# Kernel optimization log

Hardware: AMD Instinct MI355X
Metric: run time of the kernel (lower is better)

Reference implementation:

```python
import jax, jax.numpy as jnp
import numpy as np

N, E, D, L, V = 200000, 500000, 128, 5, 8
BN_EPS = 1e-5


def _bn(h, g, b, m, v):
    # eval-mode BatchNorm1d with running stats
    return (h - m) * jax.lax.rsqrt(v + BN_EPS) * g + b


def setup_inputs() -> dict:
    key = jax.random.key(0)
    ks = iter(jax.random.split(key, 40))
    nk = lambda: next(ks)
    f = lambda shape: jax.random.normal(nk(), shape, jnp.float32) * 0.05
    inp = {}
    inp["x"] = jax.random.normal(nk(), (N, 12), jnp.float32)
    inp["edge_index"] = jax.random.randint(nk(), (2, E), 0, N, dtype=jnp.int32)
    inp["edge_attr"] = jax.random.randint(nk(), (E, 3), 0, V, dtype=jnp.int32)
    # atom encoder: Lin(12,D) -> BN -> ReLU -> Lin(D,D) -> BN -> ReLU -> Lin(D,D)
    inp["ae_W1"] = f((12, D)); inp["ae_b1"] = jnp.zeros((D,), jnp.float32)
    inp["ae_g1"] = jnp.ones((D,), jnp.float32); inp["ae_be1"] = jnp.zeros((D,), jnp.float32)
    inp["ae_m1"] = f((D,)); inp["ae_v1"] = jax.random.uniform(nk(), (D,), jnp.float32) + 0.5
    inp["ae_W2"] = f((D, D)); inp["ae_b2"] = jnp.zeros((D,), jnp.float32)
    inp["ae_g2"] = jnp.ones((D,), jnp.float32); inp["ae_be2"] = jnp.zeros((D,), jnp.float32)
    inp["ae_m2"] = f((D,)); inp["ae_v2"] = jax.random.uniform(nk(), (D,), jnp.float32) + 0.5
    inp["ae_W3"] = f((D, D)); inp["ae_b3"] = jnp.zeros((D,), jnp.float32)
    # per-layer GIN params (stacked over L)
    inp["bond_emb"] = f((L, 3, V, D))
    inp["eps"] = jnp.zeros((L,), jnp.float32)
    inp["mlp_W1"] = f((L, D, D)); inp["mlp_b1"] = jnp.zeros((L, D), jnp.float32)
    inp["mlp_g"] = jnp.ones((L, D), jnp.float32); inp["mlp_be"] = jnp.zeros((L, D), jnp.float32)
    inp["mlp_m"] = f((L, D)); inp["mlp_v"] = jax.random.uniform(nk(), (L, D), jnp.float32) + 0.5
    inp["mlp_W2"] = f((L, D, D)); inp["mlp_b2"] = jnp.zeros((L, D), jnp.float32)
    # per-layer outer BatchNorm
    inp["out_g"] = jnp.ones((L, D), jnp.float32); inp["out_be"] = jnp.zeros((L, D), jnp.float32)
    inp["out_m"] = f((L, D)); inp["out_v"] = jax.random.uniform(nk(), (L, D), jnp.float32) + 0.5
    return inp


def reference(x, edge_index, edge_attr,
              ae_W1, ae_b1, ae_g1, ae_be1, ae_m1, ae_v1,
              ae_W2, ae_b2, ae_g2, ae_be2, ae_m2, ae_v2,
              ae_W3, ae_b3,
              bond_emb, eps, mlp_W1, mlp_b1, mlp_g, mlp_be, mlp_m, mlp_v,
              mlp_W2, mlp_b2, out_g, out_be, out_m, out_v):
    n_nodes = x.shape[0]
    src, dst = edge_index[0], edge_index[1]
    # atom encoder
    h = jax.nn.relu(_bn(x @ ae_W1 + ae_b1, ae_g1, ae_be1, ae_m1, ae_v1))
    h = jax.nn.relu(_bn(h @ ae_W2 + ae_b2, ae_g2, ae_be2, ae_m2, ae_v2))
    h = h @ ae_W3 + ae_b3  # [N, D]
    n_layers = bond_emb.shape[0]
    for l in range(n_layers):
        # BondEncoder: sum of per-feature embeddings -> [E, D]
        be = bond_emb[l]
        e_emb = be[0][edge_attr[:, 0]] + be[1][edge_attr[:, 1]] + be[2][edge_attr[:, 2]]
        # message: relu(x_j + edge_emb); aggregate: scatter-add at dst
        msg = jax.nn.relu(h[src] + e_emb)
        agg = jax.ops.segment_sum(msg, dst, num_segments=n_nodes)
        z = (1.0 + eps[l]) * h + agg
        # GIN MLP: Lin -> BN -> ReLU -> Lin
        z = jax.nn.relu(_bn(z @ mlp_W1[l] + mlp_b1[l], mlp_g[l], mlp_be[l], mlp_m[l], mlp_v[l]))
        z = z @ mlp_W2[l] + mlp_b2[l]
        # outer BatchNorm; ReLU on all but last layer (dropout is identity in eval)
        z = _bn(z, out_g[l], out_be[l], out_m[l], out_v[l])
        if l < n_layers - 1:
            z = jax.nn.relu(z)
        h = z
    return h  # JK='last'
```

## Files before the change

### kernel.cpp

```cpp
#include <hip/hip_runtime.h>
#include <hip/hip_bf16.h>
#include <cstdint>
#include <cstddef>

#define D 128
#define NNODES 200000
#define NEDGES 500000
#define NLAYERS 5
#define BN_EPS 1e-5f
#define MAXDEG 24

typedef __attribute__((ext_vector_type(8))) short bf16x8;
typedef __attribute__((ext_vector_type(4))) float f32x4;

__device__ __forceinline__ unsigned short f2bf(float f) {
    union { float f; unsigned int u; } x; x.f = f;
    unsigned int r = (x.u + 0x7FFFu + ((x.u >> 16) & 1u)) >> 16;
    return (unsigned short)r;
}
__device__ __forceinline__ float bf2f(unsigned short u) {
    union { unsigned int u; float f; } x; x.u = ((unsigned int)u) << 16; return x.f;
}

__global__ void k_zero(int* __restrict__ p, int n) {
    int i = blockIdx.x * 256 + threadIdx.x;
    if (i < n) p[i] = 0;
}

__global__ void k_fill_edges(const int* __restrict__ ei, const int* __restrict__ ea,
                             int* __restrict__ deg, int* __restrict__ elist, int n_edges) {
    int e = blockIdx.x * 256 + threadIdx.x;
    if (e >= n_edges) return;
    int dst = ei[n_edges + e];
    int src = ei[e];
    int a0 = ea[e * 3], a1 = ea[e * 3 + 1], a2 = ea[e * 3 + 2];
    int rec = src | (a0 << 18) | (a1 << 21) | (a2 << 24);
    int pos = atomicAdd(&deg[dst], 1);
    if (pos < MAXDEG) elist[dst * MAXDEG + pos] = rec;
}

__global__ void k_prep_w(const float* __restrict__ aeW2, const float* __restrict__ aeW3,
                         const float* __restrict__ mlpW1, const float* __restrict__ mlpW2,
                         unsigned short* __restrict__ wbt) {
    int m = blockIdx.x >> 3;
    int s = (blockIdx.x & 7) * 256 + threadIdx.x;
    int f = s >> 4;
    int kc = (s & 15) * 8;
    const float* W;
    if (m == 0) W = aeW2;
    else if (m == 1) W = aeW3;
    else if (m < 7) W = mlpW1 + (size_t)(m - 2) * D * D;
    else W = mlpW2 + (size_t)(m - 7) * D * D;
    unsigned short tmp[8];
#pragma unroll
    for (int j = 0; j < 8; ++j) tmp[j] = f2bf(W[(size_t)(kc + j) * D + f]);
    *(int4*)(wbt + (size_t)m * D * D + (size_t)f * D + kc) = *(int4*)tmp;
}

__global__ void k_bondsum(const float* __restrict__ bond, float* __restrict__ bsum) {
    int idx = blockIdx.x;
    int l = idx >> 9, combo = idx & 511;
    int a0 = combo & 7, a1 = (combo >> 3) & 7, a2 = (combo >> 6) & 7;
    int f = threadIdx.x;
    const float* bl = bond + (size_t)l * 3 * 8 * 128;
    bsum[(size_t)idx * 128 + f] =
        bl[a0 * 128 + f] + bl[1024 + a1 * 128 + f] + bl[2048 + a2 * 128 + f];
}

__global__ void k_ae1(const float* __restrict__ x, const float* __restrict__ W,
                      const float* __restrict__ b, const float* __restrict__ g,
                      const float* __restrict__ be, const float* __restrict__ m,
                      const float* __restrict__ v, unsigned short* __restrict__ out) {
    __shared__ float sW[12][128];
    int tid = threadIdx.x;
    for (int i = tid; i < 12 * 128; i += 256) sW[i >> 7][i & 127] = W[i];
    int f0 = (tid & 31) * 4;
    int g8 = tid >> 5;
    float4 bb = *(const float4*)(b + f0);
    float4 gg = *(const float4*)(g + f0);
    float4 ee = *(const float4*)(be + f0);
    float4 mm = *(const float4*)(m + f0);
    float4 vv = *(const float4*)(v + f0);
    float A0 = gg.x * rsqrtf(vv.x + BN_EPS), S0 = (bb.x - mm.x) * A0 + ee.x;
    float A1 = gg.y * rsqrtf(vv.y + BN_EPS), S1 = (bb.y - mm.y) * A1 + ee.y;
    float A2 = gg.z * rsqrtf(vv.z + BN_EPS), S2 = (bb.z - mm.z) * A2 + ee.z;
    float A3 = gg.w * rsqrtf(vv.w + BN_EPS), S3 = (bb.w - mm.w) * A3 + ee.w;
    __syncthreads();
    for (int n = blockIdx.x * 8 + g8; n < NNODES; n += gridDim.x * 8) {
        const float4* xr = (const float4*)(x + (size_t)n * 12);
        float4 x0 = xr[0], x1 = xr[1], x2 = xr[2];
        float xv[12] = {x0.x, x0.y, x0.z, x0.w, x1.x, x1.y, x1.z, x1.w,
                        x2.x, x2.y, x2.z, x2.w};
        float a0 = 0.f, a1 = 0.f, a2 = 0.f, a3 = 0.f;
#pragma unroll
        for (int k = 0; k < 12; ++k) {
            float4 wv = *(float4*)&sW[k][f0];
            a0 += xv[k] * wv.x; a1 += xv[k] * wv.y;
            a2 += xv[k] * wv.z; a3 += xv[k] * wv.w;
        }
        unsigned short o[4];
        o[0] = f2bf(fmaxf(a0 * A0 + S0, 0.f));
        o[1] = f2bf(fmaxf(a1 * A1 + S1, 0.f));
        o[2] = f2bf(fmaxf(a2 * A2 + S2, 0.f));
        o[3] = f2bf(fmaxf(a3 * A3 + S3, 0.f));
        *(uint2*)(out + (size_t)n * D + f0) = *(uint2*)o;
    }
}

__global__ void k_agg(const unsigned short* __restrict__ hin,
                      const float* __restrict__ bsum,
                      const float* __restrict__ eps_arr, int layer,
                      const int* __restrict__ deg, const int* __restrict__ elist,
                      unsigned short* __restrict__ out) {
    int tid = threadIdx.x;
    int f4 = tid & 31;
    int n = blockIdx.x * 8 + (tid >> 5);
    float epsv = 1.f + eps_arr[layer];
    ushort4 hs = *(const ushort4*)(hin + (size_t)n * D + f4 * 4);
    float z0 = epsv * bf2f(hs.x), z1 = epsv * bf2f(hs.y);
    float z2 = epsv * bf2f(hs.z), z3 = epsv * bf2f(hs.w);
    int dgr = min(deg[n], MAXDEG);
    int rec = (f4 < MAXDEG) ? elist[(size_t)n * MAXDEG + f4] : 0;
    for (int base = 0; base < dgr; base += 4) {
        int rr[4];
#pragma unroll
        for (int j = 0; j < 4; ++j) rr[j] = __shfl(rec, base + j, 32);
        ushort4 hv[4]; float4 bv[4];
#pragma unroll
        for (int j = 0; j < 4; ++j) {
            if (base + j < dgr) {
                hv[j] = *(const ushort4*)(hin + (size_t)(rr[j] & 0x3FFFF) * D + f4 * 4);
                bv[j] = *(const float4*)(bsum + (size_t)((rr[j] >> 18) & 511) * D + f4 * 4);
            }
        }
#pragma unroll
        for (int j = 0; j < 4; ++j) {
            if (base + j < dgr) {
                z0 += fmaxf(bf2f(hv[j].x) + bv[j].x, 0.f);
                z1 += fmaxf(bf2f(hv[j].y) + bv[j].y, 0.f);
                z2 += fmaxf(bf2f(hv[j].z) + bv[j].z, 0.f);
                z3 += fmaxf(bf2f(hv[j].w) + bv[j].w, 0.f);
            }
        }
    }
    unsigned short o[4] = {f2bf(z0), f2bf(z1), f2bf(z2), f2bf(z3)};
    *(uint2*)(out + (size_t)n * D + f4 * 4) = *(uint2*)o;
}

#define SWZ(row, bytecol) (((row) * 256 + (bytecol)) ^ (((row) & 7) << 4))
template<int OUTF32>
__launch_bounds__(512, 4)
__global__ void k_mlp2(const unsigned short* __restrict__ hin,
                       const unsigned short* __restrict__ W1t,
                       const float* __restrict__ b1,
                       const float* __restrict__ g1, const float* __restrict__ be1,
                       const float* __restrict__ m1, const float* __restrict__ v1,
                       const unsigned short* __restrict__ W2t,
                       const float* __restrict__ b2,
                       const float* __restrict__ g2, const float* __restrict__ be2,
                       const float* __restrict__ m2, const float* __restrict__ v2,
                       unsigned short* __restrict__ outb, float* __restrict__ outf,
                       int do_bn2, int do_relu2) {
    __shared__ char lds[65536];
    char* sW = lds;
    char* sA = lds + 32768;
    int tid = threadIdx.x;
    size_t nb = (size_t)blockIdx.x * 128;

#pragma unroll
    for (int i = 0; i < 4; ++i) {
        int s = tid + i * 512;
        int r = s >> 4, cc = (s & 15) * 16;
        int4 av = *(const int4*)((const char*)hin + (nb + r) * 256 + cc);
        *(int4*)(sA + SWZ(r, cc)) = av;
        int4 wv = *(const int4*)((const char*)W1t + r * 256 + cc);
        *(int4*)(sW + SWZ(r, cc)) = wv;
    }
    __syncthreads();

    int lane = tid & 63;
    int w = tid >> 6;
    int arow = lane & 15;
    int kq = (lane >> 4) * 8;
    int c = w * 16 + arow;

    f32x4 acc[8];
#pragma unroll
    for (int rt = 0; rt < 8; ++rt) acc[rt] = (f32x4){0.f, 0.f, 0.f, 0.f};
#pragma unroll
    for (int kb = 0; kb < 4; ++kb) {
        int k0 = kb * 32 + kq;
        bf16x8 bf = *(bf16x8*)(sW + SWZ(c, k0 * 2));
#pragma unroll
        for (int rt = 0; rt < 8; ++rt) {
            bf16x8 a = *(bf16x8*)(sA + SWZ(rt * 16 + arow, k0 * 2));
            acc[rt] = __builtin_amdgcn_mfma_f32_16x16x32_bf16(a, bf, acc[rt], 0, 0, 0);
        }
    }
    __syncthreads();

    {
        float sc = g1[c] * rsqrtf(v1[c] + BN_EPS);
        float sh = (b1[c] - m1[c]) * sc + be1[c];
#pragma unroll
        for (int rt = 0; rt < 8; ++rt) {
#pragma unroll
            for (int r = 0; r < 4; ++r) {
                int row = rt * 16 + (lane >> 4) * 4 + r;
                float z = fmaxf(acc[rt][r] * sc + sh, 0.f);
                *(unsigned short*)(sA + SWZ(row, c * 2)) = f2bf(z);
            }
        }
    }
#pragma unroll
    for (int i = 0; i < 4; ++i) {
        int s = tid + i * 512;
        int r = s >> 4, cc = (s & 15) * 16;
        *(int4*)(sW + SWZ(r, cc)) = *(const int4*)((const char*)W2t + r * 256 + cc);
    }
    __syncthreads();

#pragma unroll
    for (int rt = 0; rt < 8; ++rt) acc[rt] = (f32x4){0.f, 0.f, 0.f, 0.f};
#pragma unroll
    for (int kb = 0; kb < 4; ++kb) {
        int k0 = kb * 32 + kq;
        bf16x8 bf = *(bf16x8*)(sW + SWZ(c, k0 * 2));
#pragma unroll
        for (int rt = 0; rt < 8; ++rt) {
            bf16x8 a = *(bf16x8*)(sA + SWZ(rt * 16 + arow, k0 * 2));
            acc[rt] = __builtin_amdgcn_mfma_f32_16x16x32_bf16(a, bf, acc[rt], 0, 0, 0);
        }
    }

    float sc2 = 1.f, sh2;
    if (do_bn2) { sc2 = g2[c] * rsqrtf(v2[c] + BN_EPS); sh2 = (b2[c] - m2[c]) * sc2 + be2[c]; }
    else sh2 = b2[c];
    if constexpr (OUTF32) {
#pragma unroll
        for (int rt = 0; rt < 8; ++rt) {
#pragma unroll
            for (int r = 0; r < 4; ++r) {
                int row = rt * 16 + (lane >> 4) * 4 + r;
                float z = acc[rt][r] * sc2 + sh2;
                if (do_relu2) z = fmaxf(z, 0.f);
                if (nb + row < NNODES) outf[(nb + row) * D + c] = z;
            }
        }
    } else {
        __syncthreads();
#pragma unroll
        for (int rt = 0; rt < 8; ++rt) {
#pragma unroll
            for (int r = 0; r < 4; ++r) {
                int row = rt * 16 + (lane >> 4) * 4 + r;
                float z = acc[rt][r] * sc2 + sh2;
                if (do_relu2) z = fmaxf(z, 0.f);
                *(unsigned short*)(sW + SWZ(row, c * 2)) = f2bf(z);
            }
        }
        __syncthreads();
#pragma unroll
        for (int i = 0; i < 4; ++i) {
            int s = tid + i * 512;
            int r = s >> 4, cc = (s & 15) * 16;
            if (nb + r < NNODES)
                *(int4*)((char*)outb + (nb + r) * 256 + cc) = *(int4*)(sW + SWZ(r, cc));
        }
    }
}

extern "C" void kernel_launch(void* const* d_in, const int* in_sizes, int n_in,
                              void* d_out, int out_size, void* d_ws, size_t ws_size,
                              hipStream_t stream) {
    const float* x      = (const float*)d_in[0];
    const int*   ei     = (const int*)d_in[1];
    const int*   ea     = (const int*)d_in[2];
    const float* aeW1   = (const float*)d_in[3];
    const float* aeb1   = (const float*)d_in[4];
    const float* aeg1   = (const float*)d_in[5];
    const float* aebe1  = (const float*)d_in[6];
    const float* aem1   = (const float*)d_in[7];
    const float* aev1   = (const float*)d_in[8];
    const float* aeW2   = (const float*)d_in[9];
    const float* aeb2   = (const float*)d_in[10];
    const float* aeg2   = (const float*)d_in[11];
    const float* aebe2  = (const float*)d_in[12];
    const float* aem2   = (const float*)d_in[13];
    const float* aev2   = (const float*)d_in[14];
    const float* aeW3   = (const float*)d_in[15];
    const float* aeb3   = (const float*)d_in[16];
    const float* bond   = (const float*)d_in[17];
    const float* eps    = (const float*)d_in[18];
    const float* mlpW1  = (const float*)d_in[19];
    const float* mlpb1  = (const float*)d_in[20];
    const float* mlpg   = (const float*)d_in[21];
    const float* mlpbe  = (const float*)d_in[22];
    const float* mlpm   = (const float*)d_in[23];
    const float* mlpv   = (const float*)d_in[24];
    const float* mlpW2  = (const float*)d_in[25];
    const float* mlpb2  = (const float*)d_in[26];
    const float* outg   = (const float*)d_in[27];
    const float* outbe  = (const float*)d_in[28];
    const float* outm   = (const float*)d_in[29];
    const float* outv   = (const float*)d_in[30];

    char* ws = (char*)d_ws;
    unsigned short* hA  = (unsigned short*)ws;
    unsigned short* hB  = (unsigned short*)(ws + 51200000);
    int*   deg   = (int*)(ws + 102400000);
    int*   elist = (int*)(ws + 103200000);
    unsigned short* wbt = (unsigned short*)(ws + 122400000);
    float* bsum  = (float*)(ws + 122793216);
    float* outF = (float*)d_out;

    k_zero<<<(NNODES + 255) / 256, 256, 0, stream>>>(deg, NNODES);
    k_fill_edges<<<(NEDGES + 255) / 256, 256, 0, stream>>>(ei, ea, deg, elist, NEDGES);
    k_prep_w<<<96, 256, 0, stream>>>(aeW2, aeW3, mlpW1, mlpW2, wbt);
    k_bondsum<<<NLAYERS * 512, 128, 0, stream>>>(bond, bsum);

    k_ae1<<<1280, 256, 0, stream>>>(x, aeW1, aeb1, aeg1, aebe1, aem1, aev1, hA);
    dim3 gg((NNODES + 127) / 128);
    k_mlp2<0><<<gg, 512, 0, stream>>>(hA,
        wbt + 0 * 16384, aeb2, aeg2, aebe2, aem2, aev2,
        wbt + 1 * 16384, aeb3, aeb3, aeb3, aeb3, aeb3,
        hB, nullptr, 0, 0);

    unsigned short* hc = hB;
    for (int l = 0; l < NLAYERS; ++l) {
        unsigned short* ho = (hc == hB) ? hA : hB;
        const unsigned short* W1 = wbt + (size_t)(2 + l) * 16384;
        const unsigned short* W2 = wbt + (size_t)(7 + l) * 16384;
        k_agg<<<NNODES / 8, 256, 0, stream>>>(hc, bsum + (size_t)l * 512 * 128,
                                              eps, l, deg, elist, ho);
        if (l < NLAYERS - 1) {
            k_mlp2<0><<<gg, 512, 0, stream>>>(ho,
                W1, mlpb1 + (size_t)l * D, mlpg + (size_t)l * D, mlpbe + (size_t)l * D,
                mlpm + (size_t)l * D, mlpv + (size_t)l * D,
                W2, mlpb2 + (size_t)l * D, outg + (size_t)l * D, outbe + (size_t)l * D,
                outm + (size_t)l * D, outv + (size_t)l * D,
                ho, nullptr, 1, 1);
            hc = ho;
        } else {
            k_mlp2<1><<<gg, 512, 0, stream>>>(ho,
                W1, mlpb1 + (size_t)l * D, mlpg + (size_t)l * D, mlpbe + (size_t)l * D,
                mlpm + (size_t)l * D, mlpv + (size_t)l * D,
                W2, mlpb2 + (size_t)l * D, outg + (size_t)l * D, outbe + (size_t)l * D,
                outm + (size_t)l * D, outv + (size_t)l * D,
                nullptr, outF, 1, 0);
        }
    }
    (void)in_sizes; (void)n_in; (void)out_size; (void)ws_size;
}
```

Before: 490.5 us.

## Keep MLP weights in registers, shrink row tile to 64, prefetch more neighbors

Result: no change. 481.5 us (-1.8%).

```diff
diff --git a/kernel.cpp b/kernel.cpp
--- a/kernel.cpp
+++ b/kernel.cpp
@@ -107,6 +107,7 @@
     }
 }
 
+__launch_bounds__(256, 7)
 __global__ void k_agg(const unsigned short* __restrict__ hin,
                       const float* __restrict__ bsum,
                       const float* __restrict__ eps_arr, int layer,
@@ -115,31 +116,48 @@
     int tid = threadIdx.x;
     int f4 = tid & 31;
     int n = blockIdx.x * 8 + (tid >> 5);
+    int dgr = min(deg[n], MAXDEG);
+    int rec = (f4 < MAXDEG) ? elist[(size_t)n * MAXDEG + f4] : 0;
     float epsv = 1.f + eps_arr[layer];
     ushort4 hs = *(const ushort4*)(hin + (size_t)n * D + f4 * 4);
     float z0 = epsv * bf2f(hs.x), z1 = epsv * bf2f(hs.y);
     float z2 = epsv * bf2f(hs.z), z3 = epsv * bf2f(hs.w);
-    int dgr = min(deg[n], MAXDEG);
-    int rec = (f4 < MAXDEG) ? elist[(size_t)n * MAXDEG + f4] : 0;
-    for (int base = 0; base < dgr; base += 4) {
-        int rr[4];
-#pragma unroll
-        for (int j = 0; j < 4; ++j) rr[j] = __shfl(rec, base + j, 32);
-        ushort4 hv[4]; float4 bv[4];
+
+    ushort4 hv[6]; float4 bv[6]; int rr[6];
+#pragma unroll
+    for (int j = 0; j < 6; ++j) {
+        rr[j] = __shfl(rec, j, 32);
+        if (j < dgr) {
+            hv[j] = *(const ushort4*)(hin + (size_t)(rr[j] & 0x3FFFF) * D + f4 * 4);
+            bv[j] = *(const float4*)(bsum + (size_t)((rr[j] >> 18) & 511) * D + f4 * 4);
+        }
+    }
+#pragma unroll
+    for (int j = 0; j < 6; ++j) {
+        if (j < dgr) {
+            z0 += fmaxf(bf2f(hv[j].x) + bv[j].x, 0.f);
+            z1 += fmaxf(bf2f(hv[j].y) + bv[j].y, 0.f);
+            z2 += fmaxf(bf2f(hv[j].z) + bv[j].z, 0.f);
+            z3 += fmaxf(bf2f(hv[j].w) + bv[j].w, 0.f);
+        }
+    }
+    for (int base = 6; base < dgr; base += 4) {
+        ushort4 hw[4]; float4 bw[4]; int rt[4];
+#pragma unroll
+        for (int j = 0; j < 4; ++j) {
+            rt[j] = __shfl(rec, base + j, 32);
+            if (base + j < dgr) {
+                hw[j] = *(const ushort4*)(hin + (size_t)(rt[j] & 0x3FFFF) * D + f4 * 4);
+                bw[j] = *(const float4*)(bsum + (size_t)((rt[j] >> 18) & 511) * D + f4 * 4);
+            }
+        }
 #pragma unroll
         for (int j = 0; j < 4; ++j) {
             if (base + j < dgr) {
-                hv[j] = *(const ushort4*)(hin + (size_t)(rr[j] & 0x3FFFF) * D + f4 * 4);
-                bv[j] = *(const float4*)(bsum + (size_t)((rr[j] >> 18) & 511) * D + f4 * 4);
-            }
-        }
-#pragma unroll
-        for (int j = 0; j < 4; ++j) {
-            if (base + j < dgr) {
-                z0 += fmaxf(bf2f(hv[j].x) + bv[j].x, 0.f);
-                z1 += fmaxf(bf2f(hv[j].y) + bv[j].y, 0.f);
-                z2 += fmaxf(bf2f(hv[j].z) + bv[j].z, 0.f);
-                z3 += fmaxf(bf2f(hv[j].w) + bv[j].w, 0.f);
+                z0 += fmaxf(bf2f(hw[j].x) + bw[j].x, 0.f);
+                z1 += fmaxf(bf2f(hw[j].y) + bw[j].y, 0.f);
+                z2 += fmaxf(bf2f(hw[j].z) + bw[j].z, 0.f);
+                z3 += fmaxf(bf2f(hw[j].w) + bw[j].w, 0.f);
             }
         }
     }
@@ -149,7 +167,7 @@
 
 #define SWZ(row, bytecol) (((row) * 256 + (bytecol)) ^ (((row) & 7) << 4))
 template<int OUTF32>
-__launch_bounds__(512, 4)
+__launch_bounds__(512, 6)
 __global__ void k_mlp2(const unsigned short* __restrict__ hin,
                        const unsigned short* __restrict__ W1t,
                        const float* __restrict__ b1,
@@ -161,40 +179,39 @@
                        const float* __restrict__ m2, const float* __restrict__ v2,
                        unsigned short* __restrict__ outb, float* __restrict__ outf,
                        int do_bn2, int do_relu2) {
-    __shared__ char lds[65536];
-    char* sW = lds;
-    char* sA = lds + 32768;
+    __shared__ char sA[16384];
     int tid = threadIdx.x;
-    size_t nb = (size_t)blockIdx.x * 128;
-
-#pragma unroll
-    for (int i = 0; i < 4; ++i) {
-        int s = tid + i * 512;
-        int r = s >> 4, cc = (s & 15) * 16;
-        int4 av = *(const int4*)((const char*)hin + (nb + r) * 256 + cc);
-        *(int4*)(sA + SWZ(r, cc)) = av;
-        int4 wv = *(const int4*)((const char*)W1t + r * 256 + cc);
-        *(int4*)(sW + SWZ(r, cc)) = wv;
-    }
-    __syncthreads();
-
+    size_t nb = (size_t)blockIdx.x * 64;
     int lane = tid & 63;
     int w = tid >> 6;
     int arow = lane & 15;
     int kq = (lane >> 4) * 8;
     int c = w * 16 + arow;
 
-    f32x4 acc[8];
-#pragma unroll
-    for (int rt = 0; rt < 8; ++rt) acc[rt] = (f32x4){0.f, 0.f, 0.f, 0.f};
+    bf16x8 w1f[4], w2f[4];
+#pragma unroll
+    for (int kb = 0; kb < 4; ++kb) {
+        w1f[kb] = *(const bf16x8*)(W1t + (size_t)c * D + kb * 32 + kq);
+        w2f[kb] = *(const bf16x8*)(W2t + (size_t)c * D + kb * 32 + kq);
+    }
+#pragma unroll
+    for (int i = 0; i < 2; ++i) {
+        int s = tid + i * 512;
+        int r = s >> 4, cc = (s & 15) * 16;
+        *(int4*)(sA + SWZ(r, cc)) = *(const int4*)((const char*)hin + (nb + r) * 256 + cc);
+    }
+    __syncthreads();
+
+    f32x4 acc[4];
+#pragma unroll
+    for (int rt = 0; rt < 4; ++rt) acc[rt] = (f32x4){0.f, 0.f, 0.f, 0.f};
 #pragma unroll
     for (int kb = 0; kb < 4; ++kb) {
         int k0 = kb * 32 + kq;
-        bf16x8 bf = *(bf16x8*)(sW + SWZ(c, k0 * 2));
-#pragma unroll
-        for (int rt = 0; rt < 8; ++rt) {
+#pragma unroll
+        for (int rt = 0; rt < 4; ++rt) {
             bf16x8 a = *(bf16x8*)(sA + SWZ(rt * 16 + arow, k0 * 2));
-            acc[rt] = __builtin_amdgcn_mfma_f32_16x16x32_bf16(a, bf, acc[rt], 0, 0, 0);
+            acc[rt] = __builtin_amdgcn_mfma_f32_16x16x32_bf16(a, w1f[kb], acc[rt], 0, 0, 0);
         }
     }
     __syncthreads();
@@ -203,7 +220,7 @@
         float sc = g1[c] * rsqrtf(v1[c] + BN_EPS);
         float sh = (b1[c] - m1[c]) * sc + be1[c];
 #pragma unroll
-        for (int rt = 0; rt < 8; ++rt) {
+        for (int rt = 0; rt < 4; ++rt) {
 #pragma unroll
             for (int r = 0; r < 4; ++r) {
                 int row = rt * 16 + (lane >> 4) * 4 + r;
@@ -212,24 +229,17 @@
             }
         }
     }
-#pragma unroll
-    for (int i = 0; i < 4; ++i) {
-        int s = tid + i * 512;
-        int r = s >> 4, cc = (s & 15) * 16;
-        *(int4*)(sW + SWZ(r, cc)) = *(const int4*)((const char*)W2t + r * 256 + cc);
-    }
     __syncthreads();
 
 #pragma unroll
-    for (int rt = 0; rt < 8; ++rt) acc[rt] = (f32x4){0.f, 0.f, 0.f, 0.f};
+    for (int rt = 0; rt < 4; ++rt) acc[rt] = (f32x4){0.f, 0.f, 0.f, 0.f};
 #pragma unroll
     for (int kb = 0; kb < 4; ++kb) {
         int k0 = kb * 32 + kq;
-        bf16x8 bf = *(bf16x8*)(sW + SWZ(c, k0 * 2));
-#pragma unroll
-        for (int rt = 0; rt < 8; ++rt) {
+#pragma unroll
+        for (int rt = 0; rt < 4; ++rt) {
             bf16x8 a = *(bf16x8*)(sA + SWZ(rt * 16 + arow, k0 * 2));
-            acc[rt] = __builtin_amdgcn_mfma_f32_16x16x32_bf16(a, bf, acc[rt], 0, 0, 0);
+            acc[rt] = __builtin_amdgcn_mfma_f32_16x16x32_bf16(a, w2f[kb], acc[rt], 0, 0, 0);
         }
     }
 
@@ -238,34 +248,33 @@
     else sh2 = b2[c];
     if constexpr (OUTF32) {
 #pragma unroll
-        for (int rt = 0; rt < 8; ++rt) {
+        for (int rt = 0; rt < 4; ++rt) {
 #pragma unroll
             for (int r = 0; r < 4; ++r) {
                 int row = rt * 16 + (lane >> 4) * 4 + r;
                 float z = acc[rt][r] * sc2 + sh2;
                 if (do_relu2) z = fmaxf(z, 0.f);
-                if (nb + row < NNODES) outf[(nb + row) * D + c] = z;
+                outf[(nb + row) * D + c] = z;
             }
         }
     } else {
         __syncthreads();
 #pragma unroll
-        for (int rt = 0; rt < 8; ++rt) {
+        for (int rt = 0; rt < 4; ++rt) {
 #pragma unroll
             for (int r = 0; r < 4; ++r) {
                 int row = rt * 16 + (lane >> 4) * 4 + r;
                 float z = acc[rt][r] * sc2 + sh2;
                 if (do_relu2) z = fmaxf(z, 0.f);
-                *(unsigned short*)(sW + SWZ(row, c * 2)) = f2bf(z);
+                *(unsigned short*)(sA + SWZ(row, c * 2)) = f2bf(z);
             }
         }
         __syncthreads();
 #pragma unroll
-        for (int i = 0; i < 4; ++i) {
+        for (int i = 0; i < 2; ++i) {
             int s = tid + i * 512;
             int r = s >> 4, cc = (s & 15) * 16;
-            if (nb + r < NNODES)
-                *(int4*)((char*)outb + (nb + r) * 256 + cc) = *(int4*)(sW + SWZ(r, cc));
+            *(int4*)((char*)outb + (nb + r) * 256 + cc) = *(int4*)(sA + SWZ(r, cc));
         }
     }
 }
@@ -320,7 +329,7 @@
     k_bondsum<<<NLAYERS * 512, 128, 0, stream>>>(bond, bsum);
 
     k_ae1<<<1280, 256, 0, stream>>>(x, aeW1, aeb1, aeg1, aebe1, aem1, aev1, hA);
-    dim3 gg((NNODES + 127) / 128);
+    dim3 gg(NNODES / 64);
     k_mlp2<0><<<gg, 512, 0, stream>>>(hA,
         wbt + 0 * 16384, aeb2, aeg2, aebe2, aem2, aev2,
         wbt + 1 * 16384, aeb3, aeb3, aeb3, aeb3, aeb3,
```
